# Kernel optimization log

Hardware: AMD Instinct MI355X
Metric: run time of the kernel (lower is better)

Reference implementation:

```python
import jax, jax.numpy as jnp
import numpy as np

N = 100000   # nodes
E = 400000   # edges
L = 128      # latent_size
LN_EPS = 1e-5


def _mlp(x, W1, b1, W2, b2, g=None, beta=None):
    # build_mlp_d: Linear -> ReLU -> Linear, optional trailing LayerNorm
    h = jax.nn.relu(x @ W1 + b1)
    y = h @ W2 + b2
    if g is not None:
        mu = y.mean(-1, keepdims=True)
        var = y.var(-1, keepdims=True)
        y = (y - mu) / jnp.sqrt(var + LN_EPS) * g + beta
    return y


def setup_inputs():
    key = jax.random.key(0)
    ks = iter(jax.random.split(key, 100))

    def nrm(shape, scale=1.0):
        return jax.random.normal(next(ks), shape, jnp.float32) * scale

    inp = {}
    inp["edge_index"] = jax.random.randint(next(ks), (2, E), 0, N, dtype=jnp.int32)
    for nm in ["senders_pos", "receivers_pos", "edge_dx", "edge_dt",
               "vector_a", "vector_b", "vector_c",
               "senders_v_t", "senders_v_tm1", "senders_w_t",
               "receivers_v_t", "receivers_v_tm1", "receivers_w_t"]:
        inp[nm] = nrm((E, 3))
    inp["edge_attr"] = nrm((E, 1))
    inp["node_latent"] = nrm((N, L))

    def mlp_p(pref, din, dh, dout, ln):
        inp[pref + "_W1"] = nrm((din, dh), 1.0 / np.sqrt(din))
        inp[pref + "_b1"] = jnp.zeros((dh,), jnp.float32)
        inp[pref + "_W2"] = nrm((dh, dout), 1.0 / np.sqrt(dh))
        inp[pref + "_b2"] = jnp.zeros((dout,), jnp.float32)
        if ln:
            inp[pref + "_g"] = jnp.ones((dout,), jnp.float32)
            inp[pref + "_b"] = jnp.zeros((dout,), jnp.float32)

    mlp_p("ef", 9, L, L, True)       # edge_feat_encoder
    mlp_p("ee", 3, L, L, True)       # edge_encoder
    mlp_p("ie", 3 * L, L, L, True)   # interaction_encoder
    mlp_p("i1", L, L, 3, False)      # i1_decoder
    mlp_p("i2", L, L, 3, False)      # i2_decoder
    mlp_p("fs", L, L, 1, False)      # f_scaler
    mlp_p("nw", L, L, 1, False)      # node_weight_decoder
    mlp_p("mi", L, L, 1, False)      # m_inv_decoder
    mlp_p("ii", L, L, 1, False)      # i_inv_decoder
    mlp_p("de", L, L, 1, False)      # dv_ext_decoder
    # bias node weights to ~1 so the r0ij denominator stays away from 0
    inp["nw_b2"] = jnp.ones((1,), jnp.float32)
    return inp


def reference(edge_index, senders_pos, receivers_pos, edge_dx, edge_dt, edge_attr,
              vector_a, vector_b, vector_c,
              senders_v_t, senders_v_tm1, senders_w_t,
              receivers_v_t, receivers_v_tm1, receivers_w_t, node_latent,
              ef_W1, ef_b1, ef_W2, ef_b2, ef_g, ef_b,
              ee_W1, ee_b1, ee_W2, ee_b2, ee_g, ee_b,
              ie_W1, ie_b1, ie_W2, ie_b2, ie_g, ie_b,
              i1_W1, i1_b1, i1_W2, i1_b2,
              i2_W1, i2_b1, i2_W2, i2_b2,
              fs_W1, fs_b1, fs_W2, fs_b2,
              nw_W1, nw_b1, nw_W2, nw_b2,
              mi_W1, mi_b1, mi_W2, mi_b2,
              ii_W1, ii_b1, ii_W2, ii_b2,
              de_W1, de_b1, de_W2, de_b2):
    senders, receivers = edge_index[0], edge_index[1]

    def dots(v):  # [E,3] dotted against the three edge-frame basis vectors -> [E,3]
        return jnp.stack([jnp.einsum('ej,ej->e', v, vector_a),
                          jnp.einsum('ej,ej->e', v, vector_b),
                          jnp.einsum('ej,ej->e', v, vector_c)], axis=1)

    # --- InteractionEncoder ---
    senders_features = jnp.concatenate(
        [dots(senders_v_t), dots(senders_v_tm1), dots(senders_w_t)], axis=1)   # [E,9]
    receivers_features = -jnp.concatenate(
        [dots(receivers_v_t), dots(receivers_v_tm1), dots(receivers_w_t)], axis=1)  # [E,9]

    edge_in = jnp.concatenate(
        [jnp.linalg.norm(edge_dx, axis=1, keepdims=True),
         jnp.linalg.norm(edge_dt, axis=1, keepdims=True),
         edge_attr], axis=1)                                                    # [E,3]
    edge_latent = _mlp(edge_in, ee_W1, ee_b1, ee_W2, ee_b2, ee_g, ee_b)
    senders_latent = _mlp(senders_features, ef_W1, ef_b1, ef_W2, ef_b2, ef_g, ef_b)
    receivers_latent = _mlp(receivers_features, ef_W1, ef_b1, ef_W2, ef_b2, ef_g, ef_b)

    interaction_in = jnp.concatenate(
        [senders_latent + receivers_latent,
         node_latent[senders] + node_latent[receivers],
         edge_latent], axis=1)                                                  # [E,3L]
    interaction_latent = _mlp(interaction_in, ie_W1, ie_b1, ie_W2, ie_b2, ie_g, ie_b)

    # --- InteractionDecoder ---
    coeff_f = _mlp(interaction_latent, i1_W1, i1_b1, i1_W2, i1_b2)  # [E,3]
    coeff_a = _mlp(interaction_latent, i2_W1, i2_b1, i2_W2, i2_b2)  # [E,3]
    node_weights = _mlp(node_latent, nw_W1, nw_b1, nw_W2, nw_b2)    # [N,1]
    lambda_ij = _mlp(interaction_latent, fs_W1, fs_b1, fs_W2, fs_b2)  # [E,1]

    fij = coeff_f[:, 0:1] * vector_a + coeff_f[:, 1:2] * vector_b + coeff_f[:, 2:3] * vector_c
    aij = coeff_a[:, 0:1] * vector_a + coeff_a[:, 1:2] * vector_b + coeff_a[:, 2:3] * vector_c
    ws = node_weights[senders]
    wr = node_weights[receivers]
    r0ij = (ws * senders_pos + wr * receivers_pos) / (ws + wr)
    tauij = aij - jnp.cross(receivers_pos - r0ij, fij) * lambda_ij

    # --- Node_Internal_Dv_Decoder ---
    m_inv = _mlp(node_latent, mi_W1, mi_b1, mi_W2, mi_b2)  # [N,1]
    i_inv = _mlp(node_latent, ii_W1, ii_b1, ii_W2, ii_b2)  # [N,1]
    out_fij = jax.ops.segment_sum(fij, receivers, num_segments=N)   # scatter_add
    node_dv_int = m_inv * out_fij + _mlp(node_latent, de_W1, de_b1, de_W2, de_b2)
    out_tij = jax.ops.segment_sum(tauij, receivers, num_segments=N)
    node_dw_int = i_inv * out_tij

    return (node_dv_int, node_dw_int, interaction_latent)
```

## Files before the change

### kernel.cpp

```cpp
#include <hip/hip_runtime.h>
#include <hip/hip_fp16.h>
#include <stdint.h>

#define E_EDGES 400000
#define N_NODES 100000

#define OW1P  ((size_t)0)
#define OW2P  ((size_t)98304)
#define OW1D  ((size_t)131072)
#define OW2D  ((size_t)229376)
#define OW1E  ((size_t)241664)
#define OW2E  ((size_t)249856)
#define OW1C  ((size_t)282624)
#define OW2C  ((size_t)290816)
#define OSLR  ((size_t)524288)
#define ONW   (OSLR + (size_t)E_EDGES * 64 * 4)
#define OMI   (ONW + (size_t)N_NODES * 4)
#define OII   (OMI + (size_t)N_NODES * 4)
#define ODE   (OII + (size_t)N_NODES * 4)
#define OFS   (ODE + (size_t)N_NODES * 4)
#define OTS   (OFS + (size_t)N_NODES * 12)
#define WSEND (OTS + (size_t)N_NODES * 12)

typedef __attribute__((ext_vector_type(8))) _Float16 f16x8;
// ... 117 lines not shown
    const float* Wh = head == 0 ? i1W1 : head == 1 ? i2W1 : fsW1;
    W1D[i] = (unsigned short)f2h(Wh[(size_t)k * 128 + ch]);
  }
  if (i < 12 * 16 * 32) {
    int kin = i & 31;
    int rest = i >> 5;
    int col = rest & 15;
    int ks = rest >> 4;
    int k = ks * 32 + kin;
    float v = 0.f;
    if (k < 128) { if (col < 3) v = i1W2[(size_t)k * 3 + col]; }
    else if (k < 256) { if (col >= 3 && col < 6) v = i2W2[(size_t)(k - 128) * 3 + (col - 3)]; }
    else { if (col == 6) v = fsW2[k - 256]; }
    W2D[i] = (unsigned short)f2h(v);
  }
  if (i < 128 * 32) {
    int kin = i & 31, c = i >> 5;
    W1E[i] = (unsigned short)(kin < 9 ? f2h(efW1[(size_t)kin * 128 + c]) : 0);
  }
  if (i < 4 * 128 * 32) {
    int kin = i & 31, c = (i >> 5) & 127, ks = i >> 12;
    W2E[i] = (unsigned short)f2h(efW2[(size_t)(ks * 32 + kin) * 128 + c]);
  }
  if (i < 128 * 32) {
    int kin = i & 31, c = i >> 5;
    W1C[i] = (unsigned short)(kin < 3 ? f2h(eeW1[(size_t)kin * 128 + c]) : 0);
  }
  if (i < 4 * 128 * 32) {
    int kin = i & 31, c = (i >> 5) & 127, ks = i >> 12;
    W2C[i] = (unsigned short)f2h(eeW2[(size_t)(ks * 32 + kin) * 128 + c]);
  }
}

#define EF_YOFF 0
#define EF_XOFF 33792
#define EF_HOFF 38912
#define EF_LDS  55296

__device__ __forceinline__ void mlp32_128(uint8_t* lds, const unsigned short* W1f,
                                          const unsigned short* W2f,
                                          const float* b1, const float* b2,
                                          int w, int l) {
  int lrow = l & 15, lk = l >> 4;
  int wc = w * 32;
  f16x8 w2f[4][2];
#pragma unroll
  for (int ks = 0; ks < 4; ++ks)
#pragma unroll
    for (int ct = 0; ct < 2; ++ct)
      w2f[ks][ct] = *(const f16x8*)(W2f + ((size_t)(ks * 128 + wc + ct * 16 + lrow) * 32 + lk * 8));
  float b1c0 = b1[wc + lrow], b1c1 = b1[wc + 16 + lrow];
  float b2c0 = b2[wc + lrow], b2c1 = b2[wc + 16 + lrow];
  f16x8 bf0 = *(const f16x8*)(W1f + ((size_t)(wc + lrow) * 32 + lk * 8));
  f16x8 bf1 = *(const f16x8*)(W1f + ((size_t)(wc + 16 + lrow) * 32 + lk * 8));

  __syncthreads();

  f32x4 acc[4][2];
#pragma unroll
  for (int rt = 0; rt < 4; ++rt) {
    int row = rt * 16 + lrow;
    f16x8 af = *(const f16x8*)(lds + EF_XOFF + (uint32_t)row * 80 + lk * 16);
    acc[rt][0] = __builtin_amdgcn_mfma_f32_16x16x32_f16(af, bf0, (f32x4){0.f,0.f,0.f,0.f}, 0, 0, 0);
    acc[rt][1] = __builtin_amdgcn_mfma_f32_16x16x32_f16(af, bf1, (f32x4){0.f,0.f,0.f,0.f}, 0, 0, 0);
  }
#pragma unroll
  for (int rt = 0; rt < 4; ++rt)
#pragma unroll
    for (int ct = 0; ct < 2; ++ct) {
      float bc = ct ? b1c1 : b1c0;
      int col = wc + ct * 16 + lrow;
#pragma unroll
      for (int q = 0; q < 4; ++q) {
        int row = rt * 16 + lk * 4 + q;
        float h = fmaxf(acc[rt][ct][q] + bc, 0.f);
        uint32_t bo = ((uint32_t)row * 256 + (uint32_t)col * 2) ^ ((uint32_t)(row & 7) << 4);
        *(unsigned short*)(lds + EF_HOFF + bo) = (unsigned short)f2h(h);
      }
    }
  __syncthreads();

  f32x4 acc2[4][2];
#pragma unroll
  for (int rt = 0; rt < 4; ++rt)
#pragma unroll
    for (int ct = 0; ct < 2; ++ct) acc2[rt][ct] = (f32x4){0.f, 0.f, 0.f, 0.f};
#pragma unroll
  for (int ks = 0; ks < 4; ++ks) {
#pragma unroll
    for (int rt = 0; rt < 4; ++rt) {
      int row = rt * 16 + lrow;
      uint32_t bo = ((uint32_t)row * 256 + (uint32_t)(ks * 64 + lk * 16)) ^ ((uint32_t)(row & 7) << 4);
      f16x8 af = *(const f16x8*)(lds + EF_HOFF + bo);
      acc2[rt][0] = __builtin_amdgcn_mfma_f32_16x16x32_f16(af, w2f[ks][0], acc2[rt][0], 0, 0, 0);
      acc2[rt][1] = __builtin_amdgcn_mfma_f32_16x16x32_f16(af, w2f[ks][1], acc2[rt][1], 0, 0, 0);
    }
  }
  float* Ys = (float*)(lds + EF_YOFF);
#pragma unroll
  for (int rt = 0; rt < 4; ++rt)
#pragma unroll
    for (int ct = 0; ct < 2; ++ct) {
      float bc = ct ? b2c1 : b2c0;
      int col = wc + ct * 16 + lrow;
#pragma unroll
      for (int q = 0; q < 4; ++q) {
        int row = rt * 16 + lk * 4 + q;
        Ys[row * 132 + col] = acc2[rt][ct][q] + bc;
      }
    }
  __syncthreads();
}

__global__ __launch_bounds__(256) void k_ee_mfma(
    const float* __restrict__ dx, const float* __restrict__ dt, const float* __restrict__ attr,
    const unsigned short* __restrict__ W1C, const unsigned short* __restrict__ W2C,
    const float* __restrict__ b1, const float* __restrict__ b2,
    const float* __restrict__ g, const float* __restrict__ be, float* __restrict__ elat) {
  __shared__ uint8_t lds[EF_LDS];
  int tid = threadIdx.x;
  int w = tid >> 6, l = tid & 63;
  int base = blockIdx.x * 64;

  if (tid < 64) {
    int e = base + tid;
    float a0 = dx[e * 3], a1v = dx[e * 3 + 1], a2 = dx[e * 3 + 2];
    float t0 = dt[e * 3], t1 = dt[e * 3 + 1], t2 = dt[e * 3 + 2];
    float f0 = sqrtf(a0 * a0 + a1v * a1v + a2 * a2);
    float f1 = sqrtf(t0 * t0 + t1 * t1 + t2 * t2);
    float f2v = attr[e];
    uint32_t* xr = (uint32_t*)(lds + EF_XOFF + (uint32_t)tid * 80);
    xr[0] = f2h(f0) | (f2h(f1) << 16);
    xr[1] = f2h(f2v);
#pragma unroll
    for (int j = 2; j < 16; ++j) xr[j] = 0;
  }

  mlp32_128(lds, W1C, W2C, b1, b2, w, l);

  float* Ys = (float*)(lds + EF_YOFF);
  float gl0 = g[l], gl1 = g[l + 64], bl0 = be[l], bl1 = be[l + 64];
#pragma unroll
  for (int r16 = 0; r16 < 16; ++r16) {
    int row = w * 16 + r16;
    float y0 = Ys[row * 132 + l], y1 = Ys[row * 132 + 64 + l];
    float s = wave_sum64(y0 + y1);
    float s2 = wave_sum64(y0 * y0 + y1 * y1);
    float mu = s * 0.0078125f;
    float var = s2 * 0.0078125f - mu * mu;
    float rstd = rsqrtf(var + 1e-5f);
    size_t o = (size_t)(base + row) * 128;
    elat[o + l] = (y0 - mu) * rstd * gl0 + bl0;
    elat[o + 64 + l] = (y1 - mu) * rstd * gl1 + bl1;
  }
}

__global__ __launch_bounds__(256) void k_ef_mfma(
    const float* __restrict__ va, const float* __restrict__ vb, const float* __restrict__ vc,
    const float* __restrict__ svt, const float* __restrict__ svtm1, const float* __restrict__ swt,
    const float* __restrict__ rvt, const float* __restrict__ rvtm1, const float* __restrict__ rwt,
    const unsigned short* __restrict__ W1E, const unsigned short* __restrict__ W2E,
    const float* __restrict__ b1, const float* __restrict__ b2,
    const float* __restrict__ g, const float* __restrict__ be, uint32_t* __restrict__ slrp) {
  __shared__ uint8_t lds[EF_LDS];
  int tid = threadIdx.x;
  int w = tid >> 6, l = tid & 63;
  int base = blockIdx.x * 32;

  if (tid < 64) {
    int row = tid;
    int e = base + (row & 31);
    bool isR = row >= 32;
    const float* p0 = isR ? rvt : svt;
    const float* p1 = isR ? rvtm1 : svtm1;
    const float* p2 = isR ? rwt : swt;
    float sgn = isR ? -1.f : 1.f;
    float ax = va[e * 3], ay = va[e * 3 + 1], az = va[e * 3 + 2];
    float bx = vb[e * 3], by = vb[e * 3 + 1], bz = vb[e * 3 + 2];
    float cx = vc[e * 3], cy = vc[e * 3 + 1], cz = vc[e * 3 + 2];
    float f[10];
    const float* ps[3] = {p0, p1, p2};
#pragma unroll
    for (int q = 0; q < 3; ++q) {
      float vx = ps[q][e * 3], vy = ps[q][e * 3 + 1], vz = ps[q][e * 3 + 2];
      f[q * 3 + 0] = sgn * (vx * ax + vy * ay + vz * az);
      f[q * 3 + 1] = sgn * (vx * bx + vy * by + vz * bz);
      f[q * 3 + 2] = sgn * (vx * cx + vy * cy + vz * cz);
    }
    f[9] = 0.f;
    uint32_t* xr = (uint32_t*)(lds + EF_XOFF + (uint32_t)row * 80);
#pragma unroll
    for (int j = 0; j < 5; ++j) xr[j] = f2h(f[2 * j]) | (f2h(f[2 * j + 1]) << 16);
#pragma unroll
    for (int j = 5; j < 16; ++j) xr[j] = 0;
  }

  mlp32_128(lds, W1E, W2E, b1, b2, w, l);

  float* Ys = (float*)(lds + EF_YOFF);
  float gl0 = g[l], gl1 = g[l + 64], bl0 = be[l], bl1 = be[l + 64];
#pragma unroll
  for (int r16 = 0; r16 < 16; ++r16) {
    int row = w * 16 + r16;
    float y0 = Ys[row * 132 + l], y1 = Ys[row * 132 + 64 + l];
    float s = wave_sum64(y0 + y1);
    float s2 = wave_sum64(y0 * y0 + y1 * y1);
    float mu = s * 0.0078125f;
    float var = s2 * 0.0078125f - mu * mu;
    float rstd = rsqrtf(var + 1e-5f);
    Ys[row * 132 + l] = (y0 - mu) * rstd * gl0 + bl0;
    Ys[row * 132 + 64 + l] = (y1 - mu) * rstd * gl1 + bl1;
  }
  __syncthreads();
  if (w < 2) {
#pragma unroll
    for (int r16 = 0; r16 < 16; ++r16) {
      int row = w * 16 + r16;
      float s0 = Ys[row * 132 + l] + Ys[(row + 32) * 132 + l];
      float s1 = Ys[row * 132 + 64 + l] + Ys[(row + 32) * 132 + 64 + l];
      slrp[(size_t)(base + row) * 64 + l] = f2h(s0) | (f2h(s1) << 16);
    }
  }
}

__global__ __launch_bounds__(256) void k_ie_mfma(
    const int* __restrict__ ei, const float* __restrict__ NL,
    const uint32_t* __restrict__ slrp,
    const unsigned short* __restrict__ W1P, const unsigned short* __restrict__ W2P,
    const float* __restrict__ b1, const float* __restrict__ b2,
    const float* __restrict__ g, const float* __restrict__ be,
    float* __restrict__ il) {
  __shared__ uint8_t lds[65536];
  int tid = threadIdx.x;
  int w = tid >> 6, l = tid & 63;
  int lrow = l & 15, lk = l >> 4;
  int base = blockIdx.x * 64;

  int* eis = (int*)(lds + 49152);
  int* eit = eis + 64;
  if (tid < 64) {
    eis[tid] = ei[base + tid];
    eit[tid] = ei[E_EDGES + base + tid];
  }
  __syncthreads();

#pragma unroll
  for (int i = tid; i < 64 * 64; i += 256) {
    int r = i >> 6, c = i & 63;
    uint32_t bo = ((uint32_t)r * 768 + (uint32_t)c * 4) ^ ((uint32_t)(r & 7) << 4);
    *(uint32_t*)(lds + bo) = slrp[(size_t)(base + r) * 64 + c];
  }
  const float2* NL2 = (const float2*)NL;
#pragma unroll
  for (int i = tid; i < 64 * 64; i += 256) {
    int r = i >> 6, c = i & 63;
    float2 a = NL2[(size_t)eis[r] * 64 + c];
    float2 bq = NL2[(size_t)eit[r] * 64 + c];
    uint32_t p = f2h(a.x + bq.x) | (f2h(a.y + bq.y) << 16);
    uint32_t bo = ((uint32_t)r * 768 + 256u + (uint32_t)c * 4) ^ ((uint32_t)(r & 7) << 4);
    *(uint32_t*)(lds + bo) = p;
  }
  const float2* IL2 = (const float2*)il;
#pragma unroll
  for (int i = tid; i < 64 * 64; i += 256) {
    int r = i >> 6, c = i & 63;
    float2 a = IL2[(size_t)(base + r) * 64 + c];
    uint32_t p = f2h(a.x) | (f2h(a.y) << 16);
    uint32_t bo = ((uint32_t)r * 768 + 512u + (uint32_t)c * 4) ^ ((uint32_t)(r & 7) << 4);
    *(uint32_t*)(lds + bo) = p;
  }

  int wc = w * 32;
  f16x8 w2f[4][2];
#pragma unroll
  for (int ks = 0; ks < 4; ++ks)
#pragma unroll
    for (int ct = 0; ct < 2; ++ct)
      w2f[ks][ct] = *(const f16x8*)(W2P + ((size_t)(ks * 128 + wc + ct * 16 + lrow) * 32 + lk * 8));
  float b1c0 = b1[wc + lrow], b1c1 = b1[wc + 16 + lrow];
  float b2c0 = b2[wc + lrow], b2c1 = b2[wc + 16 + lrow];

  __syncthreads();

  f32x4 acc[4][2];
#pragma unroll
  for (int rt = 0; rt < 4; ++rt)
#pragma unroll
    for (int ct = 0; ct < 2; ++ct) acc[rt][ct] = (f32x4){0.f, 0.f, 0.f, 0.f};
#pragma unroll 2
  for (int ks = 0; ks < 12; ++ks) {
    f16x8 bf0 = *(const f16x8*)(W1P + ((size_t)(ks * 128 + wc + lrow) * 32 + lk * 8));
    f16x8 bf1 = *(const f16x8*)(W1P + ((size_t)(ks * 128 + wc + 16 + lrow) * 32 + lk * 8));
#pragma unroll
    for (int rt = 0; rt < 4; ++rt) {
      int row = rt * 16 + lrow;
      uint32_t bo = ((uint32_t)row * 768 + (uint32_t)(ks * 64 + lk * 16)) ^ ((uint32_t)(row & 7) << 4);
      f16x8 af = *(const f16x8*)(lds + bo);
      acc[rt][0] = __builtin_amdgcn_mfma_f32_16x16x32_f16(af, bf0, acc[rt][0], 0, 0, 0);
      acc[rt][1] = __builtin_amdgcn_mfma_f32_16x16x32_f16(af, bf1, acc[rt][1], 0, 0, 0);
    }
  }

#pragma unroll
  for (int rt = 0; rt < 4; ++rt)
#pragma unroll
    for (int ct = 0; ct < 2; ++ct) {
      float bc = ct ? b1c1 : b1c0;
      int col = wc + ct * 16 + lrow;
#pragma unroll
      for (int q = 0; q < 4; ++q) {
        int row = rt * 16 + lk * 4 + q;
        float h = fmaxf(acc[rt][ct][q] + bc, 0.f);
        uint32_t bo = ((uint32_t)row * 256 + (uint32_t)col * 2) ^ ((uint32_t)(row & 7) << 4);
        *(unsigned short*)(lds + 49152 + bo) = (unsigned short)f2h(h);
      }
    }
  __syncthreads();

  f32x4 acc2[4][2];
#pragma unroll
  for (int rt = 0; rt < 4; ++rt)
#pragma unroll
    for (int ct = 0; ct < 2; ++ct) acc2[rt][ct] = (f32x4){0.f, 0.f, 0.f, 0.f};
#pragma unroll
  for (int ks = 0; ks < 4; ++ks) {
#pragma unroll
    for (int rt = 0; rt < 4; ++rt) {
      int row = rt * 16 + lrow;
      uint32_t bo = ((uint32_t)row * 256 + (uint32_t)(ks * 64 + lk * 16)) ^ ((uint32_t)(row & 7) << 4);
      f16x8 af = *(const f16x8*)(lds + 49152 + bo);
      acc2[rt][0] = __builtin_amdgcn_mfma_f32_16x16x32_f16(af, w2f[ks][0], acc2[rt][0], 0, 0, 0);
      acc2[rt][1] = __builtin_amdgcn_mfma_f32_16x16x32_f16(af, w2f[ks][1], acc2[rt][1], 0, 0, 0);
    }
  }

  float* Ys = (float*)lds;
#pragma unroll
  for (int rt = 0; rt < 4; ++rt)
#pragma unroll
    for (int ct = 0; ct < 2; ++ct) {
      float bc = ct ? b2c1 : b2c0;
      int col = wc + ct * 16 + lrow;
#pragma unroll
      for (int q = 0; q < 4; ++q) {
        int row = rt * 16 + lk * 4 + q;
        Ys[row * 132 + col] = acc2[rt][ct][q] + bc;
      }
    }
  __syncthreads();

  float gl0 = g[l], gl1 = g[l + 64], bl0 = be[l], bl1 = be[l + 64];
#pragma unroll
  for (int r16 = 0; r16 < 16; ++r16) {
    int row = w * 16 + r16;
    float y0 = Ys[row * 132 + l], y1 = Ys[row * 132 + 64 + l];
    float s = wave_sum64(y0 + y1);
    float s2 = wave_sum64(y0 * y0 + y1 * y1);
    float mu = s * 0.0078125f;
    float var = s2 * 0.0078125f - mu * mu;
    float rstd = rsqrtf(var + 1e-5f);
    size_t o = (size_t)(base + row) * 128;
    il[o + l] = (y0 - mu) * rstd * gl0 + bl0;
    il[o + 64 + l] = (y1 - mu) * rstd * gl1 + bl1;
  }
}

__global__ __launch_bounds__(256) void k_dec_mfma(
    const int* __restrict__ ei, const float* __restrict__ il,
    const unsigned short* __restrict__ W1D, const unsigned short* __restrict__ W2D,
    const float* __restrict__ i1b1, const float* __restrict__ i2b1,
    const float* __restrict__ fsb1,
    const float* __restrict__ i1b2, const float* __restrict__ i2b2,
    const float* __restrict__ fsb2,
    const float* __restrict__ nw, const float* __restrict__ spos, const float* __restrict__ rpos,
    const float* __restrict__ va, const float* __restrict__ vb, const float* __restrict__ vc,
    float* __restrict__ fsum, float* __restrict__ tsum) {
  __shared__ uint8_t lds[65536];
  int tid = threadIdx.x;
  int w = tid >> 6, l = tid & 63;
  int lrow = l & 15, lk = l >> 4;
  int base = blockIdx.x * 64;

  const float2* IL2 = (const float2*)il;
#pragma unroll
  for (int i = tid; i < 64 * 64; i += 256) {
    int r = i >> 6, c = i & 63;
    float2 a = IL2[(size_t)(base + r) * 64 + c];
    uint32_t p = f2h(a.x) | (f2h(a.y) << 16);
    uint32_t bo = ((uint32_t)r * 256 + (uint32_t)c * 4) ^ ((uint32_t)(r & 7) << 4);
    *(uint32_t*)(lds + 49152 + bo) = p;
  }

  float b1c[6];
#pragma unroll
  for (int ct = 0; ct < 6; ++ct) {
    int c = w * 96 + ct * 16 + lrow;
    const float* bsel = (c < 128) ? i1b1 : (c < 256) ? i2b1 : fsb1;
    b1c[ct] = bsel[c & 127];
  }
  f16x8 w2f[12];
#pragma unroll
  for (int ks = 0; ks < 12; ++ks)
    w2f[ks] = *(const f16x8*)(W2D + ((size_t)(ks * 16 + lrow) * 32 + lk * 8));
  float b2c = lrow < 3 ? i1b2[lrow] : lrow < 6 ? i2b2[lrow - 3] : lrow == 6 ? fsb2[0] : 0.f;
  __syncthreads();

  f32x4 acc[4][6];
#pragma unroll
  for (int rt = 0; rt < 4; ++rt)
#pragma unroll
    for (int ct = 0; ct < 6; ++ct) acc[rt][ct] = (f32x4){0.f, 0.f, 0.f, 0.f};
#pragma unroll
  for (int ks = 0; ks < 4; ++ks) {
    f16x8 bf[6];
#pragma unroll
    for (int ct = 0; ct < 6; ++ct)
      bf[ct] = *(const f16x8*)(W1D + ((size_t)(ks * 384 + w * 96 + ct * 16 + lrow) * 32 + lk * 8));
#pragma unroll
    for (int rt = 0; rt < 4; ++rt) {
      int row = rt * 16 + lrow;
      uint32_t bo = ((uint32_t)row * 256 + (uint32_t)(ks * 64 + lk * 16)) ^ ((uint32_t)(row & 7) << 4);
      f16x8 af = *(const f16x8*)(lds + 49152 + bo);
#pragma unroll
      for (int ct = 0; ct < 6; ++ct)
        acc[rt][ct] = __builtin_amdgcn_mfma_f32_16x16x32_f16(af, bf[ct], acc[rt][ct], 0, 0, 0);
    }
  }

#pragma unroll
  for (int rt = 0; rt < 4; ++rt)
#pragma unroll
    for (int ct = 0; ct < 6; ++ct) {
      int col = w * 96 + ct * 16 + lrow;
#pragma unroll
      for (int q = 0; q < 4; ++q) {
        int row = rt * 16 + lk * 4 + q;
        float h = fmaxf(acc[rt][ct][q] + b1c[ct], 0.f);
        uint32_t bo = ((uint32_t)row * 768 + (uint32_t)col * 2) ^ ((uint32_t)(row & 7) << 4);
        *(unsigned short*)(lds + bo) = (unsigned short)f2h(h);
      }
    }
  __syncthreads();

  f32x4 acc2 = (f32x4){0.f, 0.f, 0.f, 0.f};
#pragma unroll
  for (int ks = 0; ks < 12; ++ks) {
    int row = w * 16 + lrow;
    uint32_t bo = ((uint32_t)row * 768 + (uint32_t)(ks * 64 + lk * 16)) ^ ((uint32_t)(row & 7) << 4);
    f16x8 af = *(const f16x8*)(lds + bo);
    acc2 = __builtin_amdgcn_mfma_f32_16x16x32_f16(af, w2f[ks], acc2, 0, 0, 0);
  }

  float* Ys = (float*)(lds + 49152);
#pragma unroll
  for (int q = 0; q < 4; ++q) {
    int row = w * 16 + lk * 4 + q;
    Ys[row * 17 + lrow] = acc2[q] + b2c;
  }
  __syncthreads();

  if (tid < 64) {
    int e = base + tid;
    int s = ei[e], t = ei[E_EDGES + e];
    float cf0 = Ys[tid * 17 + 0], cf1 = Ys[tid * 17 + 1], cf2 = Ys[tid * 17 + 2];
    float ca0 = Ys[tid * 17 + 3], ca1 = Ys[tid * 17 + 4], ca2 = Ys[tid * 17 + 5];
    float lam = Ys[tid * 17 + 6];
    float ax = va[e * 3], ay = va[e * 3 + 1], az = va[e * 3 + 2];
    float bx = vb[e * 3], by = vb[e * 3 + 1], bz = vb[e * 3 + 2];
    float cx = vc[e * 3], cy = vc[e * 3 + 1], cz = vc[e * 3 + 2];
    float fx = cf0 * ax + cf1 * bx + cf2 * cx;
    float fy = cf0 * ay + cf1 * by + cf2 * cy;
    float fz = cf0 * az + cf1 * bz + cf2 * cz;
    float gx = ca0 * ax + ca1 * bx + ca2 * cx;
    float gy = ca0 * ay + ca1 * by + ca2 * cy;
    float gz = ca0 * az + ca1 * bz + ca2 * cz;
    float wsn = nw[s], wrn = nw[t];
    float sx = spos[e * 3], sy = spos[e * 3 + 1], sz = spos[e * 3 + 2];
    float rx = rpos[e * 3], ry = rpos[e * 3 + 1], rz = rpos[e * 3 + 2];
    float inv = 1.f / (wsn + wrn);
    float r0x = (wsn * sx + wrn * rx) * inv;
    float r0y = (wsn * sy + wrn * ry) * inv;
    float r0z = (wsn * sz + wrn * rz) * inv;
    float ddx = rx - r0x, ddy = ry - r0y, ddz = rz - r0z;
    float cxx = ddy * fz - ddz * fy;
    float cyy = ddz * fx - ddx * fz;
    float czz = ddx * fy - ddy * fx;
    float tx = gx - cxx * lam, ty = gy - cyy * lam, tz = gz - czz * lam;
    atomicAdd(&fsum[(size_t)t * 3 + 0], fx);
    atomicAdd(&fsum[(size_t)t * 3 + 1], fy);
    atomicAdd(&fsum[(size_t)t * 3 + 2], fz);
    atomicAdd(&tsum[(size_t)t * 3 + 0], tx);
    atomicAdd(&tsum[(size_t)t * 3 + 1], ty);
    atomicAdd(&tsum[(size_t)t * 3 + 2], tz);
  }
// ... 83 lines not shown
  const float* de_b2 = (const float*)d_in[61];

  float* out = (float*)d_out;
  char* ws = (char*)d_ws;
  unsigned short* W1P = (unsigned short*)(ws + OW1P);
  unsigned short* W2P = (unsigned short*)(ws + OW2P);
  unsigned short* W1D = (unsigned short*)(ws + OW1D);
  unsigned short* W2D = (unsigned short*)(ws + OW2D);
  unsigned short* W1E = (unsigned short*)(ws + OW1E);
  unsigned short* W2E = (unsigned short*)(ws + OW2E);
  unsigned short* W1C = (unsigned short*)(ws + OW1C);
  unsigned short* W2C = (unsigned short*)(ws + OW2C);
  uint32_t* slrp = (uint32_t*)(ws + OSLR);
  float* o_nw = (float*)(ws + ONW);
  float* o_mi = (float*)(ws + OMI);
  float* o_ii = (float*)(ws + OII);
  float* o_de = (float*)(ws + ODE);
  float* fsum = (float*)(ws + OFS);
  float* tsum = (float*)(ws + OTS);
  float* il = out + 6 * N_NODES;

  hipMemsetAsync(ws + OFS, 0, (size_t)N_NODES * 24, stream);

  hipLaunchKernelGGL(k_prep, dim3(192), dim3(256), 0, stream, ie_W1, ie_W2,
                     i1_W1, i2_W1, fs_W1, i1_W2, i2_W2, fs_W2,
                     ef_W1, ef_W2, ee_W1, ee_W2,
                     W1P, W2P, W1D, W2D, W1E, W2E, W1C, W2C);

  hipLaunchKernelGGL(k_node, dim3(N_NODES / 32), dim3(256), 0, stream, NL,
                     nw_W1, nw_b1, nw_W2, nw_b2, mi_W1, mi_b1, mi_W2, mi_b2,
                     ii_W1, ii_b1, ii_W2, ii_b2, de_W1, de_b1, de_W2, de_b2,
                     o_nw, o_mi, o_ii, o_de);

  hipLaunchKernelGGL(k_ee_mfma, dim3(E_EDGES / 64), dim3(256), 0, stream, dx, dt, attr,
                     W1C, W2C, ee_b1, ee_b2, ee_g, ee_b, il);

  hipLaunchKernelGGL(k_ef_mfma, dim3(E_EDGES / 32), dim3(256), 0, stream, va, vb, vc,
                     svt, svtm1, swt, rvt, rvtm1, rwt,
                     W1E, W2E, ef_b1, ef_b2, ef_g, ef_b, slrp);

  hipLaunchKernelGGL(k_ie_mfma, dim3(E_EDGES / 64), dim3(256), 0, stream, ei, NL, slrp,
                     W1P, W2P, ie_b1, ie_b2, ie_g, ie_b, il);

  hipLaunchKernelGGL(k_dec_mfma, dim3(E_EDGES / 64), dim3(256), 0, stream, ei, il,
                     W1D, W2D, i1_b1, i2_b1, fs_b1, i1_b2, i2_b2, fs_b2,
                     o_nw, spos, rpos, va, vb, vc, fsum, tsum);

  hipLaunchKernelGGL(k_final, dim3((N_NODES + 255) / 256), dim3(256), 0, stream, o_mi, o_ii, o_de,
                     fsum, tsum, out);
}
```

Before: 1.421 ms.

## Fuse edge encoder into interaction kernel and halve per-block edge tiles

Removes the separate edge-encoder kernel and computes its MLP and LayerNorm inside the interaction-encoder kernel, keeping the result in registers and writing it straight into the LDS concat buffer. This avoids writing the 128-wide fp32 edge latent to global memory and reading it back. All edge kernels also process half as many edges per block with smaller LDS footprints, which is meant to raise occupancy. The risk is more blocks, more repeated weight-fragment loads per edge, and more register pressure in the fused kernel.

```diff
diff --git a/kernel.cpp b/kernel.cpp
--- a/kernel.cpp
+++ b/kernel.cpp
@@ -173,129 +173,9 @@
   }
 }
 
-#define EF_YOFF 0
-#define EF_XOFF 33792
-#define EF_HOFF 38912
-#define EF_LDS  55296
-
-__device__ __forceinline__ void mlp32_128(uint8_t* lds, const unsigned short* W1f,
-                                          const unsigned short* W2f,
-                                          const float* b1, const float* b2,
-                                          int w, int l) {
-  int lrow = l & 15, lk = l >> 4;
-  int wc = w * 32;
-  f16x8 w2f[4][2];
-#pragma unroll
-  for (int ks = 0; ks < 4; ++ks)
-#pragma unroll
-    for (int ct = 0; ct < 2; ++ct)
-      w2f[ks][ct] = *(const f16x8*)(W2f + ((size_t)(ks * 128 + wc + ct * 16 + lrow) * 32 + lk * 8));
-  float b1c0 = b1[wc + lrow], b1c1 = b1[wc + 16 + lrow];
-  float b2c0 = b2[wc + lrow], b2c1 = b2[wc + 16 + lrow];
-  f16x8 bf0 = *(const f16x8*)(W1f + ((size_t)(wc + lrow) * 32 + lk * 8));
-  f16x8 bf1 = *(const f16x8*)(W1f + ((size_t)(wc + 16 + lrow) * 32 + lk * 8));
-
-  __syncthreads();
-
-  f32x4 acc[4][2];
-#pragma unroll
-  for (int rt = 0; rt < 4; ++rt) {
-    int row = rt * 16 + lrow;
-    f16x8 af = *(const f16x8*)(lds + EF_XOFF + (uint32_t)row * 80 + lk * 16);
-    acc[rt][0] = __builtin_amdgcn_mfma_f32_16x16x32_f16(af, bf0, (f32x4){0.f,0.f,0.f,0.f}, 0, 0, 0);
-    acc[rt][1] = __builtin_amdgcn_mfma_f32_16x16x32_f16(af, bf1, (f32x4){0.f,0.f,0.f,0.f}, 0, 0, 0);
-  }
-#pragma unroll
-  for (int rt = 0; rt < 4; ++rt)
-#pragma unroll
-    for (int ct = 0; ct < 2; ++ct) {
-      float bc = ct ? b1c1 : b1c0;
-      int col = wc + ct * 16 + lrow;
-#pragma unroll
-      for (int q = 0; q < 4; ++q) {
-        int row = rt * 16 + lk * 4 + q;
-        float h = fmaxf(acc[rt][ct][q] + bc, 0.f);
-        uint32_t bo = ((uint32_t)row * 256 + (uint32_t)col * 2) ^ ((uint32_t)(row & 7) << 4);
-        *(unsigned short*)(lds + EF_HOFF + bo) = (unsigned short)f2h(h);
-      }
-    }
-  __syncthreads();
-
-  f32x4 acc2[4][2];
-#pragma unroll
-  for (int rt = 0; rt < 4; ++rt)
-#pragma unroll
-    for (int ct = 0; ct < 2; ++ct) acc2[rt][ct] = (f32x4){0.f, 0.f, 0.f, 0.f};
-#pragma unroll
-  for (int ks = 0; ks < 4; ++ks) {
-#pragma unroll
-    for (int rt = 0; rt < 4; ++rt) {
-      int row = rt * 16 + lrow;
-      uint32_t bo = ((uint32_t)row * 256 + (uint32_t)(ks * 64 + lk * 16)) ^ ((uint32_t)(row & 7) << 4);
-      f16x8 af = *(const f16x8*)(lds + EF_HOFF + bo);
-      acc2[rt][0] = __builtin_amdgcn_mfma_f32_16x16x32_f16(af, w2f[ks][0], acc2[rt][0], 0, 0, 0);
-      acc2[rt][1] = __builtin_amdgcn_mfma_f32_16x16x32_f16(af, w2f[ks][1], acc2[rt][1], 0, 0, 0);
-    }
-  }
-  float* Ys = (float*)(lds + EF_YOFF);
-#pragma unroll
-  for (int rt = 0; rt < 4; ++rt)
-#pragma unroll
-    for (int ct = 0; ct < 2; ++ct) {
-      float bc = ct ? b2c1 : b2c0;
-      int col = wc + ct * 16 + lrow;
-#pragma unroll
-      for (int q = 0; q < 4; ++q) {
-        int row = rt * 16 + lk * 4 + q;
-        Ys[row * 132 + col] = acc2[rt][ct][q] + bc;
-      }
-    }
-  __syncthreads();
-}
-
-__global__ __launch_bounds__(256) void k_ee_mfma(
-    const float* __restrict__ dx, const float* __restrict__ dt, const float* __restrict__ attr,
-    const unsigned short* __restrict__ W1C, const unsigned short* __restrict__ W2C,
-    const float* __restrict__ b1, const float* __restrict__ b2,
-    const float* __restrict__ g, const float* __restrict__ be, float* __restrict__ elat) {
-  __shared__ uint8_t lds[EF_LDS];
-  int tid = threadIdx.x;
-  int w = tid >> 6, l = tid & 63;
-  int base = blockIdx.x * 64;
-
-  if (tid < 64) {
-    int e = base + tid;
-    float a0 = dx[e * 3], a1v = dx[e * 3 + 1], a2 = dx[e * 3 + 2];
-    float t0 = dt[e * 3], t1 = dt[e * 3 + 1], t2 = dt[e * 3 + 2];
-    float f0 = sqrtf(a0 * a0 + a1v * a1v + a2 * a2);
-    float f1 = sqrtf(t0 * t0 + t1 * t1 + t2 * t2);
-    float f2v = attr[e];
-    uint32_t* xr = (uint32_t*)(lds + EF_XOFF + (uint32_t)tid * 80);
-    xr[0] = f2h(f0) | (f2h(f1) << 16);
-    xr[1] = f2h(f2v);
-#pragma unroll
-    for (int j = 2; j < 16; ++j) xr[j] = 0;
-  }
-
-  mlp32_128(lds, W1C, W2C, b1, b2, w, l);
-
-  float* Ys = (float*)(lds + EF_YOFF);
-  float gl0 = g[l], gl1 = g[l + 64], bl0 = be[l], bl1 = be[l + 64];
-#pragma unroll
-  for (int r16 = 0; r16 < 16; ++r16) {
-    int row = w * 16 + r16;
-    float y0 = Ys[row * 132 + l], y1 = Ys[row * 132 + 64 + l];
-    float s = wave_sum64(y0 + y1);
-    float s2 = wave_sum64(y0 * y0 + y1 * y1);
-    float mu = s * 0.0078125f;
-    float var = s2 * 0.0078125f - mu * mu;
-    float rstd = rsqrtf(var + 1e-5f);
-    size_t o = (size_t)(base + row) * 128;
-    elat[o + l] = (y0 - mu) * rstd * gl0 + bl0;
-    elat[o + 64 + l] = (y1 - mu) * rstd * gl1 + bl1;
-  }
-}
-
+#define EFY 0
+#define EFX 16896
+#define EFH 19456
 __global__ __launch_bounds__(256) void k_ef_mfma(
     const float* __restrict__ va, const float* __restrict__ vb, const float* __restrict__ vc,
     const float* __restrict__ svt, const float* __restrict__ svtm1, const float* __restrict__ swt,
@@ -303,15 +183,16 @@
     const unsigned short* __restrict__ W1E, const unsigned short* __restrict__ W2E,
     const float* __restrict__ b1, const float* __restrict__ b2,
     const float* __restrict__ g, const float* __restrict__ be, uint32_t* __restrict__ slrp) {
-  __shared__ uint8_t lds[EF_LDS];
+  __shared__ uint8_t lds[27648];
   int tid = threadIdx.x;
   int w = tid >> 6, l = tid & 63;
-  int base = blockIdx.x * 32;
-
-  if (tid < 64) {
+  int lrow = l & 15, lk = l >> 4;
+  int base = blockIdx.x * 16;
+
+  if (tid < 32) {
     int row = tid;
-    int e = base + (row & 31);
-    bool isR = row >= 32;
+    int e = base + (row & 15);
+    bool isR = row >= 16;
     const float* p0 = isR ? rvt : svt;
     const float* p1 = isR ? rvtm1 : svtm1;
     const float* p2 = isR ? rwt : swt;
@@ -329,20 +210,85 @@
       f[q * 3 + 2] = sgn * (vx * cx + vy * cy + vz * cz);
     }
     f[9] = 0.f;
-    uint32_t* xr = (uint32_t*)(lds + EF_XOFF + (uint32_t)row * 80);
+    uint32_t* xr = (uint32_t*)(lds + EFX + (uint32_t)row * 80);
 #pragma unroll
     for (int j = 0; j < 5; ++j) xr[j] = f2h(f[2 * j]) | (f2h(f[2 * j + 1]) << 16);
 #pragma unroll
     for (int j = 5; j < 16; ++j) xr[j] = 0;
   }
 
-  mlp32_128(lds, W1E, W2E, b1, b2, w, l);
-
-  float* Ys = (float*)(lds + EF_YOFF);
+  int wc = w * 32;
+  f16x8 w2f[4][2];
+#pragma unroll
+  for (int ks = 0; ks < 4; ++ks)
+#pragma unroll
+    for (int ct = 0; ct < 2; ++ct)
+      w2f[ks][ct] = *(const f16x8*)(W2E + ((size_t)(ks * 128 + wc + ct * 16 + lrow) * 32 + lk * 8));
+  float b1c0 = b1[wc + lrow], b1c1 = b1[wc + 16 + lrow];
+  float b2c0 = b2[wc + lrow], b2c1 = b2[wc + 16 + lrow];
+  f16x8 bf0 = *(const f16x8*)(W1E + ((size_t)(wc + lrow) * 32 + lk * 8));
+  f16x8 bf1 = *(const f16x8*)(W1E + ((size_t)(wc + 16 + lrow) * 32 + lk * 8));
+  __syncthreads();
+
+  f32x4 a1[2][2];
+#pragma unroll
+  for (int rt = 0; rt < 2; ++rt) {
+    int row = rt * 16 + lrow;
+    f16x8 af = *(const f16x8*)(lds + EFX + (uint32_t)row * 80 + lk * 16);
+    a1[rt][0] = __builtin_amdgcn_mfma_f32_16x16x32_f16(af, bf0, (f32x4){0.f,0.f,0.f,0.f}, 0, 0, 0);
+    a1[rt][1] = __builtin_amdgcn_mfma_f32_16x16x32_f16(af, bf1, (f32x4){0.f,0.f,0.f,0.f}, 0, 0, 0);
+  }
+#pragma unroll
+  for (int rt = 0; rt < 2; ++rt)
+#pragma unroll
+    for (int ct = 0; ct < 2; ++ct) {
+      float bc = ct ? b1c1 : b1c0;
+      int col = wc + ct * 16 + lrow;
+#pragma unroll
+      for (int q = 0; q < 4; ++q) {
+        int row = rt * 16 + lk * 4 + q;
+        float h = fmaxf(a1[rt][ct][q] + bc, 0.f);
+        uint32_t bo = ((uint32_t)row * 256 + (uint32_t)col * 2) ^ ((uint32_t)(row & 7) << 4);
+        *(unsigned short*)(lds + EFH + bo) = (unsigned short)f2h(h);
+      }
+    }
+  __syncthreads();
+
+  f32x4 a2[2][2];
+#pragma unroll
+  for (int rt = 0; rt < 2; ++rt)
+#pragma unroll
+    for (int ct = 0; ct < 2; ++ct) a2[rt][ct] = (f32x4){0.f, 0.f, 0.f, 0.f};
+#pragma unroll
+  for (int ks = 0; ks < 4; ++ks) {
+#pragma unroll
+    for (int rt = 0; rt < 2; ++rt) {
+      int row = rt * 16 + lrow;
+      uint32_t bo = ((uint32_t)row * 256 + (uint32_t)(ks * 64 + lk * 16)) ^ ((uint32_t)(row & 7) << 4);
+      f16x8 af = *(const f16x8*)(lds + EFH + bo);
+      a2[rt][0] = __builtin_amdgcn_mfma_f32_16x16x32_f16(af, w2f[ks][0], a2[rt][0], 0, 0, 0);
+      a2[rt][1] = __builtin_amdgcn_mfma_f32_16x16x32_f16(af, w2f[ks][1], a2[rt][1], 0, 0, 0);
+    }
+  }
+  float* Ys = (float*)(lds + EFY);
+#pragma unroll
+  for (int rt = 0; rt < 2; ++rt)
+#pragma unroll
+    for (int ct = 0; ct < 2; ++ct) {
+      float bc = ct ? b2c1 : b2c0;
+      int col = wc + ct * 16 + lrow;
+#pragma unroll
+      for (int q = 0; q < 4; ++q) {
+        int row = rt * 16 + lk * 4 + q;
+        Ys[row * 132 + col] = a2[rt][ct][q] + bc;
+      }
+    }
+  __syncthreads();
+
   float gl0 = g[l], gl1 = g[l + 64], bl0 = be[l], bl1 = be[l + 64];
 #pragma unroll
-  for (int r16 = 0; r16 < 16; ++r16) {
-    int row = w * 16 + r16;
+  for (int r8 = 0; r8 < 8; ++r8) {
+    int row = w * 8 + r8;
     float y0 = Ys[row * 132 + l], y1 = Ys[row * 132 + 64 + l];
     float s = wave_sum64(y0 + y1);
     float s2 = wave_sum64(y0 * y0 + y1 * y1);
@@ -355,63 +301,165 @@
   __syncthreads();
   if (w < 2) {
 #pragma unroll
-    for (int r16 = 0; r16 < 16; ++r16) {
-      int row = w * 16 + r16;
-      float s0 = Ys[row * 132 + l] + Ys[(row + 32) * 132 + l];
-      float s1 = Ys[row * 132 + 64 + l] + Ys[(row + 32) * 132 + 64 + l];
+    for (int r8 = 0; r8 < 8; ++r8) {
+      int row = w * 8 + r8;
+      float s0 = Ys[row * 132 + l] + Ys[(row + 16) * 132 + l];
+      float s1 = Ys[row * 132 + 64 + l] + Ys[(row + 16) * 132 + 64 + l];
       slrp[(size_t)(base + row) * 64 + l] = f2h(s0) | (f2h(s1) << 16);
     }
   }
 }
 
-__global__ __launch_bounds__(256) void k_ie_mfma(
+#define XI 0
+#define HH 24576
+#define XE 32768
+#define EIX 35328
+__global__ __launch_bounds__(256) void k_ie_fused(
     const int* __restrict__ ei, const float* __restrict__ NL,
     const uint32_t* __restrict__ slrp,
+    const float* __restrict__ dxp, const float* __restrict__ dtp, const float* __restrict__ attr,
+    const unsigned short* __restrict__ W1C, const unsigned short* __restrict__ W2C,
+    const float* __restrict__ eb1, const float* __restrict__ eb2,
+    const float* __restrict__ eg, const float* __restrict__ ebe,
     const unsigned short* __restrict__ W1P, const unsigned short* __restrict__ W2P,
     const float* __restrict__ b1, const float* __restrict__ b2,
     const float* __restrict__ g, const float* __restrict__ be,
     float* __restrict__ il) {
-  __shared__ uint8_t lds[65536];
+  __shared__ uint8_t lds[35584];
   int tid = threadIdx.x;
   int w = tid >> 6, l = tid & 63;
   int lrow = l & 15, lk = l >> 4;
-  int base = blockIdx.x * 64;
-
-  int* eis = (int*)(lds + 49152);
-  int* eit = eis + 64;
-  if (tid < 64) {
+  int base = blockIdx.x * 32;
+  int wc = w * 32;
+
+  int* eis = (int*)(lds + EIX);
+  int* eit = eis + 32;
+  if (tid < 32) {
     eis[tid] = ei[base + tid];
     eit[tid] = ei[E_EDGES + base + tid];
-  }
-  __syncthreads();
-
-#pragma unroll
-  for (int i = tid; i < 64 * 64; i += 256) {
+    int e = base + tid;
+    float a0 = dxp[e * 3], a1v = dxp[e * 3 + 1], a2 = dxp[e * 3 + 2];
+    float t0 = dtp[e * 3], t1 = dtp[e * 3 + 1], t2 = dtp[e * 3 + 2];
+    float f0 = sqrtf(a0 * a0 + a1v * a1v + a2 * a2);
+    float f1 = sqrtf(t0 * t0 + t1 * t1 + t2 * t2);
+    float f2v = attr[e];
+    uint32_t* xr = (uint32_t*)(lds + XE + (uint32_t)tid * 80);
+    xr[0] = f2h(f0) | (f2h(f1) << 16);
+    xr[1] = f2h(f2v);
+#pragma unroll
+    for (int j = 2; j < 16; ++j) xr[j] = 0;
+  }
+
+  f16x8 w2fe[4][2];
+#pragma unroll
+  for (int ks = 0; ks < 4; ++ks)
+#pragma unroll
+    for (int ct = 0; ct < 2; ++ct)
+      w2fe[ks][ct] = *(const f16x8*)(W2C + ((size_t)(ks * 128 + wc + ct * 16 + lrow) * 32 + lk * 8));
+  float eb1c0 = eb1[wc + lrow], eb1c1 = eb1[wc + 16 + lrow];
+  float eb2c0 = eb2[wc + lrow], eb2c1 = eb2[wc + 16 + lrow];
+  f16x8 bfe0 = *(const f16x8*)(W1C + ((size_t)(wc + lrow) * 32 + lk * 8));
+  f16x8 bfe1 = *(const f16x8*)(W1C + ((size_t)(wc + 16 + lrow) * 32 + lk * 8));
+  __syncthreads();
+
+  f32x4 aE[2][2];
+#pragma unroll
+  for (int rt = 0; rt < 2; ++rt) {
+    int row = rt * 16 + lrow;
+    f16x8 af = *(const f16x8*)(lds + XE + (uint32_t)row * 80 + lk * 16);
+    aE[rt][0] = __builtin_amdgcn_mfma_f32_16x16x32_f16(af, bfe0, (f32x4){0.f,0.f,0.f,0.f}, 0, 0, 0);
+    aE[rt][1] = __builtin_amdgcn_mfma_f32_16x16x32_f16(af, bfe1, (f32x4){0.f,0.f,0.f,0.f}, 0, 0, 0);
+  }
+#pragma unroll
+  for (int rt = 0; rt < 2; ++rt)
+#pragma unroll
+    for (int ct = 0; ct < 2; ++ct) {
+      float bc = ct ? eb1c1 : eb1c0;
+      int col = wc + ct * 16 + lrow;
+#pragma unroll
+      for (int q = 0; q < 4; ++q) {
+        int row = rt * 16 + lk * 4 + q;
+        float h = fmaxf(aE[rt][ct][q] + bc, 0.f);
+        uint32_t bo = ((uint32_t)row * 256 + (uint32_t)col * 2) ^ ((uint32_t)(row & 7) << 4);
+        *(unsigned short*)(lds + HH + bo) = (unsigned short)f2h(h);
+      }
+    }
+  __syncthreads();
+
+  f32x4 aE2[2][2];
+#pragma unroll
+  for (int rt = 0; rt < 2; ++rt)
+#pragma unroll
+    for (int ct = 0; ct < 2; ++ct) aE2[rt][ct] = (f32x4){0.f, 0.f, 0.f, 0.f};
+#pragma unroll
+  for (int ks = 0; ks < 4; ++ks) {
+#pragma unroll
+    for (int rt = 0; rt < 2; ++rt) {
+      int row = rt * 16 + lrow;
+      uint32_t bo = ((uint32_t)row * 256 + (uint32_t)(ks * 64 + lk * 16)) ^ ((uint32_t)(row & 7) << 4);
+      f16x8 af = *(const f16x8*)(lds + HH + bo);
+      aE2[rt][0] = __builtin_amdgcn_mfma_f32_16x16x32_f16(af, w2fe[ks][0], aE2[rt][0], 0, 0, 0);
+      aE2[rt][1] = __builtin_amdgcn_mfma_f32_16x16x32_f16(af, w2fe[ks][1], aE2[rt][1], 0, 0, 0);
+    }
+  }
+  float* Ys = (float*)(lds + XI);
+#pragma unroll
+  for (int rt = 0; rt < 2; ++rt)
+#pragma unroll
+    for (int ct = 0; ct < 2; ++ct) {
+      float bc = ct ? eb2c1 : eb2c0;
+      int col = wc + ct * 16 + lrow;
+#pragma unroll
+      for (int q = 0; q < 4; ++q) {
+        int row = rt * 16 + lk * 4 + q;
+        Ys[row * 132 + col] = aE2[rt][ct][q] + bc;
+      }
+    }
+  __syncthreads();
+
+  float el0[8], el1[8];
+  {
+    float gl0 = eg[l], gl1 = eg[l + 64], bl0 = ebe[l], bl1 = ebe[l + 64];
+#pragma unroll
+    for (int r8 = 0; r8 < 8; ++r8) {
+      int row = w * 8 + r8;
+      float y0 = Ys[row * 132 + l], y1 = Ys[row * 132 + 64 + l];
+      float s = wave_sum64(y0 + y1);
+      float s2 = wave_sum64(y0 * y0 + y1 * y1);
+      float mu = s * 0.0078125f;
+      float var = s2 * 0.0078125f - mu * mu;
+      float rstd = rsqrtf(var + 1e-5f);
+      el0[r8] = (y0 - mu) * rstd * gl0 + bl0;
+      el1[r8] = (y1 - mu) * rstd * gl1 + bl1;
+    }
+  }
+  __syncthreads();
+
+#pragma unroll
+  for (int i = tid; i < 32 * 64; i += 256) {
     int r = i >> 6, c = i & 63;
     uint32_t bo = ((uint32_t)r * 768 + (uint32_t)c * 4) ^ ((uint32_t)(r & 7) << 4);
-    *(uint32_t*)(lds + bo) = slrp[(size_t)(base + r) * 64 + c];
+    *(uint32_t*)(lds + XI + bo) = slrp[(size_t)(base + r) * 64 + c];
   }
   const float2* NL2 = (const float2*)NL;
 #pragma unroll
-  for (int i = tid; i < 64 * 64; i += 256) {
+  for (int i = tid; i < 32 * 64; i += 256) {
     int r = i >> 6, c = i & 63;
     float2 a = NL2[(size_t)eis[r] * 64 + c];
     float2 bq = NL2[(size_t)eit[r] * 64 + c];
     uint32_t p = f2h(a.x + bq.x) | (f2h(a.y + bq.y) << 16);
     uint32_t bo = ((uint32_t)r * 768 + 256u + (uint32_t)c * 4) ^ ((uint32_t)(r & 7) << 4);
-    *(uint32_t*)(lds + bo) = p;
-  }
-  const float2* IL2 = (const float2*)il;
-#pragma unroll
-  for (int i = tid; i < 64 * 64; i += 256) {
-    int r = i >> 6, c = i & 63;
-    float2 a = IL2[(size_t)(base + r) * 64 + c];
-    uint32_t p = f2h(a.x) | (f2h(a.y) << 16);
-    uint32_t bo = ((uint32_t)r * 768 + 512u + (uint32_t)c * 4) ^ ((uint32_t)(r & 7) << 4);
-    *(uint32_t*)(lds + bo) = p;
-  }
-
-  int wc = w * 32;
+    *(uint32_t*)(lds + XI + bo) = p;
+  }
+#pragma unroll
+  for (int r8 = 0; r8 < 8; ++r8) {
+    int row = w * 8 + r8;
+    uint32_t bo0 = ((uint32_t)row * 768 + 512u + (uint32_t)l * 2) ^ ((uint32_t)(row & 7) << 4);
+    uint32_t bo1 = ((uint32_t)row * 768 + 512u + (uint32_t)(l + 64) * 2) ^ ((uint32_t)(row & 7) << 4);
+    *(unsigned short*)(lds + XI + bo0) = (unsigned short)f2h(el0[r8]);
+    *(unsigned short*)(lds + XI + bo1) = (unsigned short)f2h(el1[r8]);
+  }
+
   f16x8 w2f[4][2];
 #pragma unroll
   for (int ks = 0; ks < 4; ++ks)
@@ -420,12 +468,11 @@
       w2f[ks][ct] = *(const f16x8*)(W2P + ((size_t)(ks * 128 + wc + ct * 16 + lrow) * 32 + lk * 8));
   float b1c0 = b1[wc + lrow], b1c1 = b1[wc + 16 + lrow];
   float b2c0 = b2[wc + lrow], b2c1 = b2[wc + 16 + lrow];
-
-  __syncthreads();
-
-  f32x4 acc[4][2];
-#pragma unroll
-  for (int rt = 0; rt < 4; ++rt)
+  __syncthreads();
+
+  f32x4 acc[2][2];
+#pragma unroll
+  for (int rt = 0; rt < 2; ++rt)
 #pragma unroll
     for (int ct = 0; ct < 2; ++ct) acc[rt][ct] = (f32x4){0.f, 0.f, 0.f, 0.f};
 #pragma unroll 2
@@ -433,17 +480,16 @@
     f16x8 bf0 = *(const f16x8*)(W1P + ((size_t)(ks * 128 + wc + lrow) * 32 + lk * 8));
     f16x8 bf1 = *(const f16x8*)(W1P + ((size_t)(ks * 128 + wc + 16 + lrow) * 32 + lk * 8));
 #pragma unroll
-    for (int rt = 0; rt < 4; ++rt) {
+    for (int rt = 0; rt < 2; ++rt) {
       int row = rt * 16 + lrow;
       uint32_t bo = ((uint32_t)row * 768 + (uint32_t)(ks * 64 + lk * 16)) ^ ((uint32_t)(row & 7) << 4);
-      f16x8 af = *(const f16x8*)(lds + bo);
+      f16x8 af = *(const f16x8*)(lds + XI + bo);
       acc[rt][0] = __builtin_amdgcn_mfma_f32_16x16x32_f16(af, bf0, acc[rt][0], 0, 0, 0);
       acc[rt][1] = __builtin_amdgcn_mfma_f32_16x16x32_f16(af, bf1, acc[rt][1], 0, 0, 0);
     }
   }
-
-#pragma unroll
-  for (int rt = 0; rt < 4; ++rt)
+#pragma unroll
+  for (int rt = 0; rt < 2; ++rt)
 #pragma unroll
     for (int ct = 0; ct < 2; ++ct) {
       float bc = ct ? b1c1 : b1c0;
@@ -453,31 +499,29 @@
         int row = rt * 16 + lk * 4 + q;
         float h = fmaxf(acc[rt][ct][q] + bc, 0.f);
         uint32_t bo = ((uint32_t)row * 256 + (uint32_t)col * 2) ^ ((uint32_t)(row & 7) << 4);
-        *(unsigned short*)(lds + 49152 + bo) = (unsigned short)f2h(h);
+        *(unsigned short*)(lds + HH + bo) = (unsigned short)f2h(h);
       }
     }
   __syncthreads();
 
-  f32x4 acc2[4][2];
-#pragma unroll
-  for (int rt = 0; rt < 4; ++rt)
+  f32x4 acc2[2][2];
+#pragma unroll
+  for (int rt = 0; rt < 2; ++rt)
 #pragma unroll
     for (int ct = 0; ct < 2; ++ct) acc2[rt][ct] = (f32x4){0.f, 0.f, 0.f, 0.f};
 #pragma unroll
   for (int ks = 0; ks < 4; ++ks) {
 #pragma unroll
-    for (int rt = 0; rt < 4; ++rt) {
+    for (int rt = 0; rt < 2; ++rt) {
       int row = rt * 16 + lrow;
       uint32_t bo = ((uint32_t)row * 256 + (uint32_t)(ks * 64 + lk * 16)) ^ ((uint32_t)(row & 7) << 4);
-      f16x8 af = *(const f16x8*)(lds + 49152 + bo);
+      f16x8 af = *(const f16x8*)(lds + HH + bo);
       acc2[rt][0] = __builtin_amdgcn_mfma_f32_16x16x32_f16(af, w2f[ks][0], acc2[rt][0], 0, 0, 0);
       acc2[rt][1] = __builtin_amdgcn_mfma_f32_16x16x32_f16(af, w2f[ks][1], acc2[rt][1], 0, 0, 0);
     }
   }
-
-  float* Ys = (float*)lds;
-#pragma unroll
-  for (int rt = 0; rt < 4; ++rt)
+#pragma unroll
+  for (int rt = 0; rt < 2; ++rt)
 #pragma unroll
     for (int ct = 0; ct < 2; ++ct) {
       float bc = ct ? b2c1 : b2c0;
@@ -492,8 +536,8 @@
 
   float gl0 = g[l], gl1 = g[l + 64], bl0 = be[l], bl1 = be[l + 64];
 #pragma unroll
-  for (int r16 = 0; r16 < 16; ++r16) {
-    int row = w * 16 + r16;
+  for (int r8 = 0; r8 < 8; ++r8) {
+    int row = w * 8 + r8;
     float y0 = Ys[row * 132 + l], y1 = Ys[row * 132 + 64 + l];
     float s = wave_sum64(y0 + y1);
     float s2 = wave_sum64(y0 * y0 + y1 * y1);
@@ -516,20 +560,20 @@
     const float* __restrict__ nw, const float* __restrict__ spos, const float* __restrict__ rpos,
     const float* __restrict__ va, const float* __restrict__ vb, const float* __restrict__ vc,
     float* __restrict__ fsum, float* __restrict__ tsum) {
-  __shared__ uint8_t lds[65536];
+  __shared__ uint8_t lds[32768];
   int tid = threadIdx.x;
   int w = tid >> 6, l = tid & 63;
   int lrow = l & 15, lk = l >> 4;
-  int base = blockIdx.x * 64;
+  int base = blockIdx.x * 32;
 
   const float2* IL2 = (const float2*)il;
 #pragma unroll
-  for (int i = tid; i < 64 * 64; i += 256) {
+  for (int i = tid; i < 32 * 64; i += 256) {
     int r = i >> 6, c = i & 63;
     float2 a = IL2[(size_t)(base + r) * 64 + c];
     uint32_t p = f2h(a.x) | (f2h(a.y) << 16);
     uint32_t bo = ((uint32_t)r * 256 + (uint32_t)c * 4) ^ ((uint32_t)(r & 7) << 4);
-    *(uint32_t*)(lds + 49152 + bo) = p;
+    *(uint32_t*)(lds + 24576 + bo) = p;
   }
 
   float b1c[6];
@@ -546,9 +590,9 @@
   float b2c = lrow < 3 ? i1b2[lrow] : lrow < 6 ? i2b2[lrow - 3] : lrow == 6 ? fsb2[0] : 0.f;
   __syncthreads();
 
-  f32x4 acc[4][6];
-#pragma unroll
-  for (int rt = 0; rt < 4; ++rt)
+  f32x4 acc[2][6];
+#pragma unroll
+  for (int rt = 0; rt < 2; ++rt)
 #pragma unroll
     for (int ct = 0; ct < 6; ++ct) acc[rt][ct] = (f32x4){0.f, 0.f, 0.f, 0.f};
 #pragma unroll
@@ -558,18 +602,17 @@
     for (int ct = 0; ct < 6; ++ct)
       bf[ct] = *(const f16x8*)(W1D + ((size_t)(ks * 384 + w * 96 + ct * 16 + lrow) * 32 + lk * 8));
 #pragma unroll
-    for (int rt = 0; rt < 4; ++rt) {
+    for (int rt = 0; rt < 2; ++rt) {
       int row = rt * 16 + lrow;
       uint32_t bo = ((uint32_t)row * 256 + (uint32_t)(ks * 64 + lk * 16)) ^ ((uint32_t)(row & 7) << 4);
-      f16x8 af = *(const f16x8*)(lds + 49152 + bo);
+      f16x8 af = *(const f16x8*)(lds + 24576 + bo);
 #pragma unroll
       for (int ct = 0; ct < 6; ++ct)
         acc[rt][ct] = __builtin_amdgcn_mfma_f32_16x16x32_f16(af, bf[ct], acc[rt][ct], 0, 0, 0);
     }
   }
-
-#pragma unroll
-  for (int rt = 0; rt < 4; ++rt)
+#pragma unroll
+  for (int rt = 0; rt < 2; ++rt)
 #pragma unroll
     for (int ct = 0; ct < 6; ++ct) {
       int col = w * 96 + ct * 16 + lrow;
@@ -583,24 +626,25 @@
     }
   __syncthreads();
 
-  f32x4 acc2 = (f32x4){0.f, 0.f, 0.f, 0.f};
-#pragma unroll
-  for (int ks = 0; ks < 12; ++ks) {
-    int row = w * 16 + lrow;
-    uint32_t bo = ((uint32_t)row * 768 + (uint32_t)(ks * 64 + lk * 16)) ^ ((uint32_t)(row & 7) << 4);
-    f16x8 af = *(const f16x8*)(lds + bo);
-    acc2 = __builtin_amdgcn_mfma_f32_16x16x32_f16(af, w2f[ks], acc2, 0, 0, 0);
-  }
-
-  float* Ys = (float*)(lds + 49152);
-#pragma unroll
-  for (int q = 0; q < 4; ++q) {
-    int row = w * 16 + lk * 4 + q;
-    Ys[row * 17 + lrow] = acc2[q] + b2c;
-  }
-  __syncthreads();
-
-  if (tid < 64) {
+  float* Ys = (float*)(lds + 24576);
+  if (w < 2) {
+    f32x4 acc2 = (f32x4){0.f, 0.f, 0.f, 0.f};
+#pragma unroll
+    for (int ks = 0; ks < 12; ++ks) {
+      int row = w * 16 + lrow;
+      uint32_t bo = ((uint32_t)row * 768 + (uint32_t)(ks * 64 + lk * 16)) ^ ((uint32_t)(row & 7) << 4);
+      f16x8 af = *(const f16x8*)(lds + bo);
+      acc2 = __builtin_amdgcn_mfma_f32_16x16x32_f16(af, w2f[ks], acc2, 0, 0, 0);
+    }
+#pragma unroll
+    for (int q = 0; q < 4; ++q) {
+      int row = w * 16 + lk * 4 + q;
+      Ys[row * 17 + lrow] = acc2[q] + b2c;
+    }
+  }
+  __syncthreads();
+
+  if (tid < 32) {
     int e = base + tid;
     int s = ei[e], t = ei[E_EDGES + e];
     float cf0 = Ys[tid * 17 + 0], cf1 = Ys[tid * 17 + 1], cf2 = Ys[tid * 17 + 2];
@@ -750,17 +794,15 @@
                      ii_W1, ii_b1, ii_W2, ii_b2, de_W1, de_b1, de_W2, de_b2,
                      o_nw, o_mi, o_ii, o_de);
 
-  hipLaunchKernelGGL(k_ee_mfma, dim3(E_EDGES / 64), dim3(256), 0, stream, dx, dt, attr,
-                     W1C, W2C, ee_b1, ee_b2, ee_g, ee_b, il);
-
-  hipLaunchKernelGGL(k_ef_mfma, dim3(E_EDGES / 32), dim3(256), 0, stream, va, vb, vc,
+  hipLaunchKernelGGL(k_ef_mfma, dim3(E_EDGES / 16), dim3(256), 0, stream, va, vb, vc,
                      svt, svtm1, swt, rvt, rvtm1, rwt,
                      W1E, W2E, ef_b1, ef_b2, ef_g, ef_b, slrp);
 
-  hipLaunchKernelGGL(k_ie_mfma, dim3(E_EDGES / 64), dim3(256), 0, stream, ei, NL, slrp,
+  hipLaunchKernelGGL(k_ie_fused, dim3(E_EDGES / 32), dim3(256), 0, stream, ei, NL, slrp,
+                     dx, dt, attr, W1C, W2C, ee_b1, ee_b2, ee_g, ee_b,
                      W1P, W2P, ie_b1, ie_b2, ie_g, ie_b, il);
 
-  hipLaunchKernelGGL(k_dec_mfma, dim3(E_EDGES / 64), dim3(256), 0, stream, ei, il,
+  hipLaunchKernelGGL(k_dec_mfma, dim3(E_EDGES / 32), dim3(256), 0, stream, ei, il,
                      W1D, W2D, i1_b1, i2_b1, fs_b1, i1_b2, i2_b2, fs_b2,
                      o_nw, spos, rpos, va, vb, vc, fsum, tsum);
 
```

After: 1.216 ms. 14.4% less time.
